# Kernel optimization log

Measured on AMD Instinct MI355X. Metric: run time of the kernel, lower is better.

Reference implementation:

```python
import jax, jax.numpy as jnp
import numpy as np

LEVEL = 3  # matches init_kwargs
# pywt Wavelet('db4').rec_lo (synthesis low-pass, 8 taps)
REC_LO = np.array([
    0.23037781330885523, 0.7148465705525415, 0.6308807679295904,
    -0.02798376941698385, -0.18703481171888114, 0.030841381835986965,
    0.032883011666982945, -0.010597401784997278], dtype=np.float32)


def _rec_filters():
    rec_lo = jnp.asarray(REC_LO)
    L = rec_lo.shape[0]
    # QMF relation: rec_hi[k] = (-1)^k * rec_lo[L-1-k]
    signs = jnp.asarray((-1.0) ** np.arange(L), dtype=rec_lo.dtype)
    rec_hi = rec_lo[::-1] * signs
    return rec_lo, rec_hi


def _iswt(coeffs, rec_lo, rec_hi):
    """Inverse stationary (undecimated / a-trous) wavelet transform.

    coeffs = [cA_L, cD_L, cD_{L-1}, ..., cD_1], each of shape [BN, T].
    Perfect reconstruction for the circular-padded dilated-conv SWT
    (ptwt/pywt convention): at each level with dilation d,
      x[n] = 0.5 * sum_m rec_lo[m]*a[(n - d*(m - L//2 + 1)) % T]
                 + rec_hi[m]*cd[(n - d*(m - L//2 + 1)) % T]
    """
    L = rec_lo.shape[0]
    n_lev = len(coeffs) - 1
    res = coeffs[0]
    for c_pos in range(n_lev):
        hi = coeffs[1 + c_pos]
        d = 2 ** (n_lev - 1 - c_pos)
        acc = jnp.zeros_like(res)
        for m in range(L):  # static 8-tap loop, unrolled under jit
            shift = d * (m - L // 2 + 1)
            acc = acc + rec_lo[m] * jnp.roll(res, shift, axis=-1) \
                      + rec_hi[m] * jnp.roll(hi, shift, axis=-1)
        res = 0.5 * acc
    return res


def setup_inputs() -> dict:
    key = jax.random.key(0)
    B, N, T = 32, 64, 4096
    x = jax.random.normal(key, (B, (LEVEL + 1) * N, T), dtype=jnp.float32)
    return {"x": x}


def reference(x):
    B, expanded_N, T = x.shape
    N = expanded_N // (LEVEL + 1)
    xr = x.reshape(B * N, LEVEL + 1, T)  # (B,N,level+1,T) merged over B,N
    coeffs = [xr[:, i, :] for i in range(LEVEL + 1)]
    rec_lo, rec_hi = _rec_filters()
    rec = _iswt(coeffs, rec_lo, rec_hi)  # [B*N, T]
    return rec.reshape(B, N, T)
```

## Files before the change

kernel.cpp:

```cpp
#include <hip/hip_runtime.h>


namespace {

constexpr int TT = 4096;
constexpr int T4 = TT / 4;
constexpr int NT = 256;

#define GLD16(gp, lp)                                                      \
  __builtin_amdgcn_global_load_lds(                                        \
      (const __attribute__((address_space(1))) void*)(gp),                 \
      (__attribute__((address_space(3))) void*)(lp), 16, 0, 0)

template <int D>
__device__ __forceinline__ void level_compute(const float* lds_res,
                                              const float* lds_hi,
                                              int t, float4 acc[4]) {
  constexpr float LO[8] = {
      0.23037781330885523f,  0.7148465705525415f,  0.6308807679295904f,
      -0.02798376941698385f, -0.18703481171888114f, 0.030841381835986965f,
      0.032883011666982945f, -0.010597401784997278f};
  constexpr float HI[8] = {
      -0.010597401784997278f, -0.032883011666982945f, 0.030841381835986965f,
      0.18703481171888114f,   -0.02798376941698385f,  -0.6308807679295904f,
      0.7148465705525415f,    -0.23037781330885523f};

  constexpr int W4 = (7 * D + 7) / 4;
  const float4* res4 = reinterpret_cast<const float4*>(lds_res);
  const float4* hir4 = reinterpret_cast<const float4*>(lds_hi);

#pragma unroll
  for (int g = 0; g < 4; ++g) {
    const int c = t + g * NT;
    float w[4 * W4];

#pragma unroll
    for (int i = 0; i < W4; ++i) {
      const float4 v = res4[(c - D + i) & (T4 - 1)];
      w[4 * i + 0] = v.x; w[4 * i + 1] = v.y;
      w[4 * i + 2] = v.z; w[4 * i + 3] = v.w;
    }
    float a0 = 0.f, a1 = 0.f, a2 = 0.f, a3 = 0.f;
#pragma unroll
    for (int m = 0; m < 8; ++m) {
      const int o = D * (7 - m);
      a0 += LO[m] * w[o + 0];
      a1 += LO[m] * w[o + 1];
      a2 += LO[m] * w[o + 2];
      a3 += LO[m] * w[o + 3];
    }

#pragma unroll
    for (int i = 0; i < W4; ++i) {
      const float4 v = hir4[(c - D + i) & (T4 - 1)];
      w[4 * i + 0] = v.x; w[4 * i + 1] = v.y;
      w[4 * i + 2] = v.z; w[4 * i + 3] = v.w;
    }
#pragma unroll
    for (int m = 0; m < 8; ++m) {
      const int o = D * (7 - m);
      a0 += HI[m] * w[o + 0];
      a1 += HI[m] * w[o + 1];
      a2 += HI[m] * w[o + 2];
      a3 += HI[m] * w[o + 3];
    }
    acc[g] = make_float4(0.5f * a0, 0.5f * a1, 0.5f * a2, 0.5f * a3);
  }
}

__global__ __launch_bounds__(NT) void iswt_kernel(const float* __restrict__ x,
                                                  float* __restrict__ out) {
  __shared__ __align__(16) float lds_res[TT];
  __shared__ __align__(16) float lds_hiA[TT];
  __shared__ __align__(16) float lds_hiB[TT];

  const int t = threadIdx.x;
  const int row = blockIdx.x;

  const float* xr = x + (size_t)row * 4 * TT;

#pragma unroll
  for (int k = 0; k < 4; ++k)
    GLD16(xr + 0 * TT + (t + k * NT) * 4, lds_res + (t + k * NT) * 4);
#pragma unroll
  for (int k = 0; k < 4; ++k)
    GLD16(xr + 1 * TT + (t + k * NT) * 4, lds_hiA + (t + k * NT) * 4);
#pragma unroll
  for (int k = 0; k < 4; ++k)
    GLD16(xr + 2 * TT + (t + k * NT) * 4, lds_hiB + (t + k * NT) * 4);

  asm volatile("s_waitcnt vmcnt(4)\n\ts_barrier" ::: "memory");

  float4 acc[4];
  float4* res4 = reinterpret_cast<float4*>(lds_res);

  level_compute<4>(lds_res, lds_hiA, t, acc);
  asm volatile("s_waitcnt lgkmcnt(0)\n\ts_barrier" ::: "memory");

#pragma unroll
  for (int k = 0; k < 4; ++k)
    GLD16(xr + 3 * TT + (t + k * NT) * 4, lds_hiA + (t + k * NT) * 4);
#pragma unroll
  for (int k = 0; k < 4; ++k) res4[t + k * NT] = acc[k];

  asm volatile("s_waitcnt vmcnt(4) lgkmcnt(0)\n\ts_barrier" ::: "memory");

  level_compute<2>(lds_res, lds_hiB, t, acc);
  asm volatile("s_waitcnt lgkmcnt(0)\n\ts_barrier" ::: "memory");

#pragma unroll
  for (int k = 0; k < 4; ++k) res4[t + k * NT] = acc[k];

  asm volatile("s_waitcnt vmcnt(0) lgkmcnt(0)\n\ts_barrier" ::: "memory");

  level_compute<1>(lds_res, lds_hiA, t, acc);
  float4* out4 = reinterpret_cast<float4*>(out) + (size_t)row * T4;
#pragma unroll
  for (int k = 0; k < 4; ++k) out4[t + k * NT] = acc[k];
}

}

extern "C" void kernel_launch(void* const* d_in, const int* in_sizes, int n_in,
                              void* d_out, int out_size, void* d_ws, size_t ws_size,
                              hipStream_t stream) {
  const float* x = reinterpret_cast<const float*>(d_in[0]);
  float* out = reinterpret_cast<float*>(d_out);
  const int rows = out_size / TT;
  iswt_kernel<<<rows, NT, 0, stream>>>(x, out);
}
```

Before: 201.2 us.

## Use 1024 threads per row with one float4 each and preload all levels

Raises the block to 1024 threads so each thread computes a single float4 per level instead of four. A fourth LDS buffer is added so all four coefficient rows are issued to LDS up front, which removes the mid-kernel reload into a reused buffer. The aim is more memory-level parallelism and shorter per-thread serial work. The cost is more LDS per block (64KB), which limits how many blocks fit on a CU, and barriers that now span 16 waves.

Measured after the change: 199.3 us. Within noise of the previous version (-1.0%).

```diff
diff --git a/kernel.cpp b/kernel.cpp
--- a/kernel.cpp
+++ b/kernel.cpp
@@ -5,7 +5,7 @@
 
 constexpr int TT = 4096;
 constexpr int T4 = TT / 4;
-constexpr int NT = 256;
+constexpr int NT = 1024;
 
 #define GLD16(gp, lp)                                                      \
   __builtin_amdgcn_global_load_lds(                                        \
@@ -13,9 +13,8 @@
       (__attribute__((address_space(3))) void*)(lp), 16, 0, 0)
 
 template <int D>
-__device__ __forceinline__ void level_compute(const float* lds_res,
-                                              const float* lds_hi,
-                                              int t, float4 acc[4]) {
+__device__ __forceinline__ float4 level_compute(const float* lds_res,
+                                                const float* lds_hi, int c) {
   constexpr float LO[8] = {
       0.23037781330885523f,  0.7148465705525415f,  0.6308807679295904f,
       -0.02798376941698385f, -0.18703481171888114f, 0.030841381835986965f,
@@ -29,94 +28,74 @@
   const float4* res4 = reinterpret_cast<const float4*>(lds_res);
   const float4* hir4 = reinterpret_cast<const float4*>(lds_hi);
 
-#pragma unroll
-  for (int g = 0; g < 4; ++g) {
-    const int c = t + g * NT;
-    float w[4 * W4];
+  float w[4 * W4];
 
 #pragma unroll
-    for (int i = 0; i < W4; ++i) {
-      const float4 v = res4[(c - D + i) & (T4 - 1)];
-      w[4 * i + 0] = v.x; w[4 * i + 1] = v.y;
-      w[4 * i + 2] = v.z; w[4 * i + 3] = v.w;
-    }
-    float a0 = 0.f, a1 = 0.f, a2 = 0.f, a3 = 0.f;
+  for (int i = 0; i < W4; ++i) {
+    const float4 v = res4[(c - D + i) & (T4 - 1)];
+    w[4 * i + 0] = v.x; w[4 * i + 1] = v.y;
+    w[4 * i + 2] = v.z; w[4 * i + 3] = v.w;
+  }
+  float a0 = 0.f, a1 = 0.f, a2 = 0.f, a3 = 0.f;
 #pragma unroll
-    for (int m = 0; m < 8; ++m) {
-      const int o = D * (7 - m);
-      a0 += LO[m] * w[o + 0];
-      a1 += LO[m] * w[o + 1];
-      a2 += LO[m] * w[o + 2];
-      a3 += LO[m] * w[o + 3];
-    }
+  for (int m = 0; m < 8; ++m) {
+    const int o = D * (7 - m);
+    a0 += LO[m] * w[o + 0];
+    a1 += LO[m] * w[o + 1];
+    a2 += LO[m] * w[o + 2];
+    a3 += LO[m] * w[o + 3];
+  }
 
 #pragma unroll
-    for (int i = 0; i < W4; ++i) {
-      const float4 v = hir4[(c - D + i) & (T4 - 1)];
-      w[4 * i + 0] = v.x; w[4 * i + 1] = v.y;
-      w[4 * i + 2] = v.z; w[4 * i + 3] = v.w;
-    }
+  for (int i = 0; i < W4; ++i) {
+    const float4 v = hir4[(c - D + i) & (T4 - 1)];
+    w[4 * i + 0] = v.x; w[4 * i + 1] = v.y;
+    w[4 * i + 2] = v.z; w[4 * i + 3] = v.w;
+  }
 #pragma unroll
-    for (int m = 0; m < 8; ++m) {
-      const int o = D * (7 - m);
-      a0 += HI[m] * w[o + 0];
-      a1 += HI[m] * w[o + 1];
-      a2 += HI[m] * w[o + 2];
-      a3 += HI[m] * w[o + 3];
-    }
-    acc[g] = make_float4(0.5f * a0, 0.5f * a1, 0.5f * a2, 0.5f * a3);
+  for (int m = 0; m < 8; ++m) {
+    const int o = D * (7 - m);
+    a0 += HI[m] * w[o + 0];
+    a1 += HI[m] * w[o + 1];
+    a2 += HI[m] * w[o + 2];
+    a3 += HI[m] * w[o + 3];
   }
+  return make_float4(0.5f * a0, 0.5f * a1, 0.5f * a2, 0.5f * a3);
 }
 
-__global__ __launch_bounds__(NT) void iswt_kernel(const float* __restrict__ x,
-                                                  float* __restrict__ out) {
+__global__ __launch_bounds__(NT, 8) void iswt_kernel(const float* __restrict__ x,
+                                                     float* __restrict__ out) {
   __shared__ __align__(16) float lds_res[TT];
-  __shared__ __align__(16) float lds_hiA[TT];
-  __shared__ __align__(16) float lds_hiB[TT];
+  __shared__ __align__(16) float lds_h3[TT];
+  __shared__ __align__(16) float lds_h2[TT];
+  __shared__ __align__(16) float lds_h1[TT];
 
   const int t = threadIdx.x;
   const int row = blockIdx.x;
 
   const float* xr = x + (size_t)row * 4 * TT;
 
-#pragma unroll
-  for (int k = 0; k < 4; ++k)
-    GLD16(xr + 0 * TT + (t + k * NT) * 4, lds_res + (t + k * NT) * 4);
-#pragma unroll
-  for (int k = 0; k < 4; ++k)
-    GLD16(xr + 1 * TT + (t + k * NT) * 4, lds_hiA + (t + k * NT) * 4);
-#pragma unroll
-  for (int k = 0; k < 4; ++k)
-    GLD16(xr + 2 * TT + (t + k * NT) * 4, lds_hiB + (t + k * NT) * 4);
+  GLD16(xr + 0 * TT + t * 4, lds_res + t * 4);
+  GLD16(xr + 1 * TT + t * 4, lds_h3 + t * 4);
+  GLD16(xr + 2 * TT + t * 4, lds_h2 + t * 4);
+  GLD16(xr + 3 * TT + t * 4, lds_h1 + t * 4);
 
-  asm volatile("s_waitcnt vmcnt(4)\n\ts_barrier" ::: "memory");
-
-  float4 acc[4];
   float4* res4 = reinterpret_cast<float4*>(lds_res);
 
-  level_compute<4>(lds_res, lds_hiA, t, acc);
+  asm volatile("s_waitcnt vmcnt(2)\n\ts_barrier" ::: "memory");
+
+  float4 acc = level_compute<4>(lds_res, lds_h3, t);
   asm volatile("s_waitcnt lgkmcnt(0)\n\ts_barrier" ::: "memory");
+  res4[t] = acc;
+  asm volatile("s_waitcnt vmcnt(1) lgkmcnt(0)\n\ts_barrier" ::: "memory");
 
-#pragma unroll
-  for (int k = 0; k < 4; ++k)
-    GLD16(xr + 3 * TT + (t + k * NT) * 4, lds_hiA + (t + k * NT) * 4);
-#pragma unroll
-  for (int k = 0; k < 4; ++k) res4[t + k * NT] = acc[k];
-
-  asm volatile("s_waitcnt vmcnt(4) lgkmcnt(0)\n\ts_barrier" ::: "memory");
-
-  level_compute<2>(lds_res, lds_hiB, t, acc);
+  acc = level_compute<2>(lds_res, lds_h2, t);
   asm volatile("s_waitcnt lgkmcnt(0)\n\ts_barrier" ::: "memory");
-
-#pragma unroll
-  for (int k = 0; k < 4; ++k) res4[t + k * NT] = acc[k];
-
+  res4[t] = acc;
   asm volatile("s_waitcnt vmcnt(0) lgkmcnt(0)\n\ts_barrier" ::: "memory");
 
-  level_compute<1>(lds_res, lds_hiA, t, acc);
-  float4* out4 = reinterpret_cast<float4*>(out) + (size_t)row * T4;
-#pragma unroll
-  for (int k = 0; k < 4; ++k) out4[t + k * NT] = acc[k];
+  acc = level_compute<1>(lds_res, lds_h1, t);
+  reinterpret_cast<float4*>(out)[(size_t)row * T4 + t] = acc;
 }
 
 }
```

## Give each thread adjacent float4 chunks with swizzled LDS and a fourth buffer

Applied to the files above, without the earlier changes.

Each thread now computes two adjacent float4 chunks with 512 threads per block, so neighbouring outputs share one loaded window and fewer LDS reads are needed per output. The LDS layout is XOR-swizzled to avoid bank conflicts when threads read contiguous chunk pairs. A fourth LDS buffer lets all four coefficient rows be prefetched up front. The final result goes back through LDS so global stores stay coalesced. The cost is more LDS per block (64KB), which may limit occupancy, plus an extra LDS round trip and a barrier at the end.

Result: faster. 196.7 us (-2.3%).

```diff
diff --git a/kernel.cpp b/kernel.cpp
--- a/kernel.cpp
+++ b/kernel.cpp
@@ -5,17 +5,23 @@
 
 constexpr int TT = 4096;
 constexpr int T4 = TT / 4;
-constexpr int NT = 256;
+constexpr int NT = 512;
+constexpr int NCH = 2;
 
 #define GLD16(gp, lp)                                                      \
   __builtin_amdgcn_global_load_lds(                                        \
       (const __attribute__((address_space(1))) void*)(gp),                 \
       (__attribute__((address_space(3))) void*)(lp), 16, 0, 0)
 
+__device__ __forceinline__ int sl(int c) {
+  c &= (T4 - 1);
+  return c ^ ((c >> 3) & 7);
+}
+
 template <int D>
 __device__ __forceinline__ void level_compute(const float* lds_res,
-                                              const float* lds_hi,
-                                              int t, float4 acc[4]) {
+                                              const float* lds_hi, int u,
+                                              float4 acc[NCH]) {
   constexpr float LO[8] = {
       0.23037781330885523f,  0.7148465705525415f,  0.6308807679295904f,
       -0.02798376941698385f, -0.18703481171888114f, 0.030841381835986965f,
@@ -25,54 +31,60 @@
       0.18703481171888114f,   -0.02798376941698385f,  -0.6308807679295904f,
       0.7148465705525415f,    -0.23037781330885523f};
 
-  constexpr int W4 = (7 * D + 7) / 4;
+  constexpr int W4 = (7 * D + 4 * NCH + 3) / 4;
   const float4* res4 = reinterpret_cast<const float4*>(lds_res);
   const float4* hir4 = reinterpret_cast<const float4*>(lds_hi);
+  const int c0 = NCH * u - D;
+
+  float w[4 * W4];
+  float a[NCH][4];
 
 #pragma unroll
-  for (int g = 0; g < 4; ++g) {
-    const int c = t + g * NT;
-    float w[4 * W4];
+  for (int i = 0; i < W4; ++i) {
+    const float4 v = res4[sl(c0 + i)];
+    w[4 * i + 0] = v.x; w[4 * i + 1] = v.y;
+    w[4 * i + 2] = v.z; w[4 * i + 3] = v.w;
+  }
+#pragma unroll
+  for (int jc = 0; jc < NCH; ++jc)
+#pragma unroll
+    for (int r = 0; r < 4; ++r) a[jc][r] = 0.f;
+#pragma unroll
+  for (int m = 0; m < 8; ++m) {
+    const int o = D * (7 - m);
+#pragma unroll
+    for (int jc = 0; jc < NCH; ++jc)
+#pragma unroll
+      for (int r = 0; r < 4; ++r) a[jc][r] += LO[m] * w[o + 4 * jc + r];
+  }
 
 #pragma unroll
-    for (int i = 0; i < W4; ++i) {
-      const float4 v = res4[(c - D + i) & (T4 - 1)];
-      w[4 * i + 0] = v.x; w[4 * i + 1] = v.y;
-      w[4 * i + 2] = v.z; w[4 * i + 3] = v.w;
-    }
-    float a0 = 0.f, a1 = 0.f, a2 = 0.f, a3 = 0.f;
+  for (int i = 0; i < W4; ++i) {
+    const float4 v = hir4[sl(c0 + i)];
+    w[4 * i + 0] = v.x; w[4 * i + 1] = v.y;
+    w[4 * i + 2] = v.z; w[4 * i + 3] = v.w;
+  }
 #pragma unroll
-    for (int m = 0; m < 8; ++m) {
-      const int o = D * (7 - m);
-      a0 += LO[m] * w[o + 0];
-      a1 += LO[m] * w[o + 1];
-      a2 += LO[m] * w[o + 2];
-      a3 += LO[m] * w[o + 3];
-    }
+  for (int m = 0; m < 8; ++m) {
+    const int o = D * (7 - m);
+#pragma unroll
+    for (int jc = 0; jc < NCH; ++jc)
+#pragma unroll
+      for (int r = 0; r < 4; ++r) a[jc][r] += HI[m] * w[o + 4 * jc + r];
+  }
 
 #pragma unroll
-    for (int i = 0; i < W4; ++i) {
-      const float4 v = hir4[(c - D + i) & (T4 - 1)];
-      w[4 * i + 0] = v.x; w[4 * i + 1] = v.y;
-      w[4 * i + 2] = v.z; w[4 * i + 3] = v.w;
-    }
-#pragma unroll
-    for (int m = 0; m < 8; ++m) {
-      const int o = D * (7 - m);
-      a0 += HI[m] * w[o + 0];
-      a1 += HI[m] * w[o + 1];
-      a2 += HI[m] * w[o + 2];
-      a3 += HI[m] * w[o + 3];
-    }
-    acc[g] = make_float4(0.5f * a0, 0.5f * a1, 0.5f * a2, 0.5f * a3);
-  }
+  for (int jc = 0; jc < NCH; ++jc)
+    acc[jc] = make_float4(0.5f * a[jc][0], 0.5f * a[jc][1],
+                          0.5f * a[jc][2], 0.5f * a[jc][3]);
 }
 
-__global__ __launch_bounds__(NT) void iswt_kernel(const float* __restrict__ x,
-                                                  float* __restrict__ out) {
+__global__ __launch_bounds__(NT, 4) void iswt_kernel(const float* __restrict__ x,
+                                                     float* __restrict__ out) {
   __shared__ __align__(16) float lds_res[TT];
-  __shared__ __align__(16) float lds_hiA[TT];
-  __shared__ __align__(16) float lds_hiB[TT];
+  __shared__ __align__(16) float lds_h3[TT];
+  __shared__ __align__(16) float lds_h2[TT];
+  __shared__ __align__(16) float lds_h1[TT];
 
   const int t = threadIdx.x;
   const int row = blockIdx.x;
@@ -80,43 +92,56 @@
   const float* xr = x + (size_t)row * 4 * TT;
 
 #pragma unroll
-  for (int k = 0; k < 4; ++k)
-    GLD16(xr + 0 * TT + (t + k * NT) * 4, lds_res + (t + k * NT) * 4);
+  for (int k = 0; k < NCH; ++k) {
+    const int s = k * NT + t;
+    GLD16(xr + 0 * TT + sl(s) * 4, lds_res + s * 4);
+  }
 #pragma unroll
-  for (int k = 0; k < 4; ++k)
-    GLD16(xr + 1 * TT + (t + k * NT) * 4, lds_hiA + (t + k * NT) * 4);
+  for (int k = 0; k < NCH; ++k) {
+    const int s = k * NT + t;
+    GLD16(xr + 1 * TT + sl(s) * 4, lds_h3 + s * 4);
+  }
 #pragma unroll
-  for (int k = 0; k < 4; ++k)
-    GLD16(xr + 2 * TT + (t + k * NT) * 4, lds_hiB + (t + k * NT) * 4);
+  for (int k = 0; k < NCH; ++k) {
+    const int s = k * NT + t;
+    GLD16(xr + 2 * TT + sl(s) * 4, lds_h2 + s * 4);
+  }
+#pragma unroll
+  for (int k = 0; k < NCH; ++k) {
+    const int s = k * NT + t;
+    GLD16(xr + 3 * TT + sl(s) * 4, lds_h1 + s * 4);
+  }
+
+  float4* res4 = reinterpret_cast<float4*>(lds_res);
+  float4 acc[NCH];
 
   asm volatile("s_waitcnt vmcnt(4)\n\ts_barrier" ::: "memory");
 
-  float4 acc[4];
-  float4* res4 = reinterpret_cast<float4*>(lds_res);
+  level_compute<4>(lds_res, lds_h3, t, acc);
+  asm volatile("s_waitcnt lgkmcnt(0)\n\ts_barrier" ::: "memory");
+#pragma unroll
+  for (int jc = 0; jc < NCH; ++jc) res4[sl(NCH * t + jc)] = acc[jc];
+  asm volatile("s_waitcnt vmcnt(2) lgkmcnt(0)\n\ts_barrier" ::: "memory");
 
-  level_compute<4>(lds_res, lds_hiA, t, acc);
+  level_compute<2>(lds_res, lds_h2, t, acc);
+  asm volatile("s_waitcnt lgkmcnt(0)\n\ts_barrier" ::: "memory");
+#pragma unroll
+  for (int jc = 0; jc < NCH; ++jc) res4[sl(NCH * t + jc)] = acc[jc];
+  asm volatile("s_waitcnt vmcnt(0) lgkmcnt(0)\n\ts_barrier" ::: "memory");
+
+  level_compute<1>(lds_res, lds_h1, t, acc);
+
+  float4* bounce4 = reinterpret_cast<float4*>(lds_h3);
+#pragma unroll
+  for (int jc = 0; jc < NCH; ++jc) bounce4[sl(NCH * t + jc)] = acc[jc];
   asm volatile("s_waitcnt lgkmcnt(0)\n\ts_barrier" ::: "memory");
 
-#pragma unroll
-  for (int k = 0; k < 4; ++k)
-    GLD16(xr + 3 * TT + (t + k * NT) * 4, lds_hiA + (t + k * NT) * 4);
-#pragma unroll
-  for (int k = 0; k < 4; ++k) res4[t + k * NT] = acc[k];
-
-  asm volatile("s_waitcnt vmcnt(4) lgkmcnt(0)\n\ts_barrier" ::: "memory");
-
-  level_compute<2>(lds_res, lds_hiB, t, acc);
-  asm volatile("s_waitcnt lgkmcnt(0)\n\ts_barrier" ::: "memory");
-
-#pragma unroll
-  for (int k = 0; k < 4; ++k) res4[t + k * NT] = acc[k];
-
-  asm volatile("s_waitcnt vmcnt(0) lgkmcnt(0)\n\ts_barrier" ::: "memory");
-
-  level_compute<1>(lds_res, lds_hiA, t, acc);
   float4* out4 = reinterpret_cast<float4*>(out) + (size_t)row * T4;
 #pragma unroll
-  for (int k = 0; k < 4; ++k) out4[t + k * NT] = acc[k];
+  for (int k = 0; k < NCH; ++k) {
+    const int c = k * NT + t;
+    out4[c] = bounce4[sl(c)];
+  }
 }
 
 }
```
